# Kernel tuning notes

Hardware: AMD Instinct MI355X
Metric: run time of the kernel (lower is better)

The kernel has to match this reference:

```python
import jax, jax.numpy as jnp
import numpy as np

N = 65536      # total atoms
D = 1024       # hidden_size (encoder output dim)
H = 2048       # ffn_hidden_size
OUT = 1        # output_size
M = 4096       # number of molecules (segments)


def _lin(k, fi, fo):
    return jax.random.normal(k, (fi, fo), jnp.float32) * (1.0 / np.sqrt(fi))


def setup_inputs() -> dict:
    key = jax.random.key(0)
    ks = jax.random.split(key, 14)
    hidden = jax.random.normal(ks[0], (N, D), jnp.float32)
    segment_ids = jnp.sort(jax.random.randint(ks[1], (N,), 0, M)).astype(jnp.int64)
    inp = {
        "hidden": hidden,
        "ffn_W1": _lin(ks[2], D, H), "ffn_b1": jnp.zeros((H,), jnp.float32),
        "ffn_W2": _lin(ks[3], H, H), "ffn_b2": jnp.zeros((H,), jnp.float32),
        "ffn_W3": _lin(ks[4], H, OUT), "ffn_b3": jnp.zeros((OUT,), jnp.float32),
        "wr_W1": _lin(ks[5], D, H), "wr_b1": jnp.zeros((H,), jnp.float32),
        "wr_W2": _lin(ks[6], H, H), "wr_b2": jnp.zeros((H,), jnp.float32),
        "wr_W3": _lin(ks[7], H, OUT), "wr_b3": jnp.ones((OUT,), jnp.float32),  # bias=1 keeps segment weight sums away from 0
        "segment_ids": segment_ids,
    }
    return inp


def _ffn(x, W1, b1, W2, b2, W3, b3):
    # Dropout(p) is identity in eval; activation = ReLU
    h = jax.nn.relu(x @ W1 + b1)
    h = jax.nn.relu(h @ W2 + b2)
    return h @ W3 + b3


def reference(hidden, ffn_W1, ffn_b1, ffn_W2, ffn_b2, ffn_W3, ffn_b3,
              wr_W1, wr_b1, wr_W2, wr_b2, wr_W3, wr_b3, segment_ids):
    seg = segment_ids.astype(jnp.int32)
    output = _ffn(hidden, ffn_W1, ffn_b1, ffn_W2, ffn_b2, ffn_W3, ffn_b3)   # [N, OUT]
    weights = _ffn(hidden, wr_W1, wr_b1, wr_W2, wr_b2, wr_W3, wr_b3)        # [N, OUT]
    # per-molecule sums over ALL elements of the segment slice (matches .sum())
    out_sum = jax.ops.segment_sum(output.sum(-1), seg, num_segments=M)      # [M]
    w_sum = jax.ops.segment_sum(weights.sum(-1), seg, num_segments=M)       # [M]
    ratio = (out_sum / w_sum)[seg][:, None]                                 # [N, 1]
    return output - weights * ratio
```

## Files before the change

### kernel.cpp

```cpp
#include <hip/hip_runtime.h>
#include <hip/hip_bf16.h>

#define DEVINL __device__ __forceinline__

typedef __attribute__((ext_vector_type(8))) short s8v;
typedef __attribute__((ext_vector_type(4))) float f4v;

using bf16 = __hip_bfloat16;

DEVINL unsigned short f2bu(float f) {
  bf16 h = __float2bfloat16(f);
  return *reinterpret_cast<unsigned short*>(&h);
}

DEVINL void gload16(const void* g, void* l) {
  __builtin_amdgcn_global_load_lds((const __attribute__((address_space(1))) void*)g,
                                   (__attribute__((address_space(3))) void*)l, 16, 0, 0);
}

__global__ void k_f32_to_bf16(const float* __restrict__ x, unsigned short* __restrict__ y, long n4) {
  long i = (long)blockIdx.x * blockDim.x + threadIdx.x;
  if (i >= n4) return;
  float4 v = ((const float4*)x)[i];
  ushort4 o;
  o.x = f2bu(v.x); o.y = f2bu(v.y); o.z = f2bu(v.z); o.w = f2bu(v.w);
  ((ushort4*)y)[i] = o;
}

__global__ void k_transpose_bf16(const float* __restrict__ W, unsigned short* __restrict__ Wt,
                                 int rows, int cols) {
  __shared__ float tile[32][33];
  const int tx = threadIdx.x, ty = threadIdx.y;
  const int c0 = blockIdx.x * 32, r0 = blockIdx.y * 32;
  #pragma unroll
  for (int i = ty; i < 32; i += 8)
    tile[i][tx] = W[(long)(r0 + i) * cols + (c0 + tx)];
  __syncthreads();
  #pragma unroll
  for (int i = ty; i < 32; i += 8)
    Wt[(long)(c0 + i) * rows + (r0 + tx)] = f2bu(tile[tx][i]);
}

template<int EPI>
__global__ __launch_bounds__(256, 2)
void k_gemm_bt(const unsigned short* __restrict__ A, const unsigned short* __restrict__ Bt,
               unsigned short* __restrict__ C, const float* __restrict__ bias,
               const float* __restrict__ w3, float* __restrict__ oacc,
               int N, int K) {
  __shared__ unsigned short As[128 * 64];
  __shared__ unsigned short Bs[128 * 64];
  const int tid = threadIdx.x;
  const int w = tid >> 6;
  const int lane = tid & 63;
  const int bn = blockIdx.x, bm = blockIdx.y;
  const int wm = (w >> 1) * 64, wn = (w & 1) * 64;

  f4v acc[4][4];
  #pragma unroll
  for (int a = 0; a < 4; ++a)
    #pragma unroll
    for (int b = 0; b < 4; ++b)
      #pragma unroll
      for (int r = 0; r < 4; ++r) acc[a][b][r] = 0.f;

  const int r_in = lane >> 3;
  const int c_in = (lane & 7) * 8;
  const unsigned short* Ag = A + ((long)bm * 128 + w * 32 + r_in) * K + c_in;
  const unsigned short* Bg = Bt + ((long)bn * 128 + w * 32 + r_in) * K + c_in;
  char* AsB = (char*)As + w * 32 * 128;
  char* BsB = (char*)Bs + w * 32 * 128;

  const int row_a = wm + (lane & 15);
  const int row_b = wn + (lane & 15);
  const int kreg = (lane >> 4) * 8;

  for (int kt = 0; kt < K; kt += 64) {
    __syncthreads();
    #pragma unroll
    for (int t = 0; t < 4; ++t) {
      gload16(Ag + (long)t * 8 * K, AsB + t * 1024);
      gload16(Bg + (long)t * 8 * K, BsB + t * 1024);
    }
    Ag += 64; Bg += 64;
    __syncthreads();
    #pragma unroll
    for (int kk = 0; kk < 2; ++kk) {
      s8v af[4], bf_[4];
      const int kb = kk * 32 + kreg;
      #pragma unroll
      for (int i = 0; i < 4; ++i) {
        af[i]  = *(const s8v*)&As[(row_a + i * 16) * 64 + kb];
        bf_[i] = *(const s8v*)&Bs[(row_b + i * 16) * 64 + kb];
      }
      #pragma unroll
      for (int mi = 0; mi < 4; ++mi)
        #pragma unroll
        for (int ni = 0; ni < 4; ++ni)
          acc[mi][ni] = __builtin_amdgcn_mfma_f32_16x16x32_bf16(af[mi], bf_[ni], acc[mi][ni], 0, 0, 0);
    }
  }

  const int crow0 = wm + (lane >> 4) * 4;
  const int ccol0 = wn + (lane & 15);
  if (EPI == 1) {
    #pragma unroll
    for (int mi = 0; mi < 4; ++mi)
      #pragma unroll
      for (int ni = 0; ni < 4; ++ni) {
        const int col = bn * 128 + ccol0 + ni * 16;
        const float bb = bias[col];
        #pragma unroll
        for (int r = 0; r < 4; ++r) {
          const long row = (long)bm * 128 + crow0 + mi * 16 + r;
          float v = acc[mi][ni][r] + bb;
          v = v > 0.f ? v : 0.f;
          C[row * N + col] = f2bu(v);
        }
      }
  } else {
    #pragma unroll
    for (int mi = 0; mi < 4; ++mi)
      #pragma unroll
      for (int r = 0; r < 4; ++r) {
        float s = 0.f;
        #pragma unroll
        for (int ni = 0; ni < 4; ++ni) {
          const int col = bn * 128 + ccol0 + ni * 16;
          float v = acc[mi][ni][r] + bias[col];
          v = v > 0.f ? v : 0.f;
          s += v * w3[col];
        }
        s += __shfl_xor(s, 1, 64);
        s += __shfl_xor(s, 2, 64);
        s += __shfl_xor(s, 4, 64);
        s += __shfl_xor(s, 8, 64);
        if ((lane & 15) == 0) {
          const long row = (long)bm * 128 + crow0 + mi * 16 + r;
          atomicAdd(&oacc[row], s);
        }
      }
  }
}

__global__ void k_detect(const int* __restrict__ seg, int n, int* __restrict__ flag) {
  if (blockIdx.x == 0 && threadIdx.x == 0) flag[0] = (seg[n - 1] == 0) ? 1 : 0;
}

__global__ void k_segsum(const float* __restrict__ oacc, const float* __restrict__ wacc,
                         const int* __restrict__ seg, const int* __restrict__ flag,
                         const float* __restrict__ ob3, const float* __restrict__ wb3,
                         float* __restrict__ osum, float* __restrict__ wsum, int n) {
  int i = blockIdx.x * blockDim.x + threadIdx.x;
  if (i >= n) return;
  int s = flag[0] ? seg[2 * i] : seg[i];
  atomicAdd(&osum[s], oacc[i] + ob3[0]);
  atomicAdd(&wsum[s], wacc[i] + wb3[0]);
}

__global__ void k_final(const float* __restrict__ oacc, const float* __restrict__ wacc,
                        const int* __restrict__ seg, const int* __restrict__ flag,
                        const float* __restrict__ ob3, const float* __restrict__ wb3,
                        const float* __restrict__ osum, const float* __restrict__ wsum,
                        float* __restrict__ out, int n) {
  int i = blockIdx.x * blockDim.x + threadIdx.x;
  if (i >= n) return;
  int s = flag[0] ? seg[2 * i] : seg[i];
  float o = oacc[i] + ob3[0];
  float ww = wacc[i] + wb3[0];
  out[i] = o - ww * (osum[s] / wsum[s]);
}

extern "C" void kernel_launch(void* const* d_in, const int* in_sizes, int n_in,
                              void* d_out, int out_size, void* d_ws, size_t ws_size,
                              hipStream_t stream) {
  constexpr int NA = 65536, D = 1024, H = 2048, M = 4096;
  const float* hidden = (const float*)d_in[0];
  const float* fW1 = (const float*)d_in[1];
  const float* fb1 = (const float*)d_in[2];
  const float* fW2 = (const float*)d_in[3];
  const float* fb2 = (const float*)d_in[4];
  const float* fW3 = (const float*)d_in[5];
  const float* fb3 = (const float*)d_in[6];
  const float* wW1 = (const float*)d_in[7];
  const float* wb1 = (const float*)d_in[8];
  const float* wW2 = (const float*)d_in[9];
  const float* wb2 = (const float*)d_in[10];
  const float* wW3 = (const float*)d_in[11];
  const float* wb3 = (const float*)d_in[12];
  const int* seg = (const int*)d_in[13];
  float* out = (float*)d_out;

  char* ws = (char*)d_ws;
  size_t off = 0;
  auto alloc = [&](size_t bytes) { char* p = ws + off; off += (bytes + 255) & ~(size_t)255; return p; };
  unsigned short* hbf  = (unsigned short*)alloc((size_t)NA * D * 2);
  unsigned short* w1tf = (unsigned short*)alloc((size_t)H * D * 2);
  unsigned short* w1tw = (unsigned short*)alloc((size_t)H * D * 2);
  unsigned short* w2tf = (unsigned short*)alloc((size_t)H * H * 2);
  unsigned short* w2tw = (unsigned short*)alloc((size_t)H * H * 2);
  unsigned short* h1   = (unsigned short*)alloc((size_t)NA * H * 2);
  float* oacc = (float*)alloc((size_t)NA * 4);
  float* wacc = (float*)alloc((size_t)NA * 4);
  float* osum = (float*)alloc((size_t)M * 4);
  float* wsum = (float*)alloc((size_t)M * 4);
  int* flag = (int*)alloc(256);

  k_f32_to_bf16<<<(int)((long)NA * D / 4 / 256), 256, 0, stream>>>(hidden, hbf, (long)NA * D / 4);
  dim3 tb(32, 8);
  k_transpose_bf16<<<dim3(H / 32, D / 32), tb, 0, stream>>>(fW1, w1tf, D, H);
  k_transpose_bf16<<<dim3(H / 32, D / 32), tb, 0, stream>>>(wW1, w1tw, D, H);
  k_transpose_bf16<<<dim3(H / 32, H / 32), tb, 0, stream>>>(fW2, w2tf, H, H);
  k_transpose_bf16<<<dim3(H / 32, H / 32), tb, 0, stream>>>(wW2, w2tw, H, H);

  hipMemsetAsync(oacc, 0, (size_t)((char*)flag - (char*)oacc), stream);
  k_detect<<<1, 64, 0, stream>>>(seg, NA, flag);

  k_gemm_bt<1><<<dim3(H / 128, NA / 128), 256, 0, stream>>>(hbf, w1tf, h1, fb1, nullptr, nullptr, H, D);
  k_gemm_bt<2><<<dim3(H / 128, NA / 128), 256, 0, stream>>>(h1, w2tf, nullptr, fb2, fW3, oacc, H, H);
  k_gemm_bt<1><<<dim3(H / 128, NA / 128), 256, 0, stream>>>(hbf, w1tw, h1, wb1, nullptr, nullptr, H, D);
  k_gemm_bt<2><<<dim3(H / 128, NA / 128), 256, 0, stream>>>(h1, w2tw, nullptr, wb2, wW3, wacc, H, H);

  k_segsum<<<NA / 256, 256, 0, stream>>>(oacc, wacc, seg, flag, fb3, wb3, osum, wsum, NA);
  k_final<<<NA / 256, 256, 0, stream>>>(oacc, wacc, seg, flag, fb3, wb3, osum, wsum, out, NA);
}
```

Measured before the change: 2.135 ms.

## Replace GEMM with 256x256 tile, 8-wave, double-buffered swizzled LDS pipeline

New measurement: 2.041 ms. -4.4%, faster.

```diff
diff --git a/kernel.cpp b/kernel.cpp
--- a/kernel.cpp
+++ b/kernel.cpp
@@ -7,10 +7,11 @@
 typedef __attribute__((ext_vector_type(4))) float f4v;
 
 using bf16 = __hip_bfloat16;
-
-DEVINL unsigned short f2bu(float f) {
+typedef unsigned short u16;
+
+DEVINL u16 f2bu(float f) {
   bf16 h = __float2bfloat16(f);
-  return *reinterpret_cast<unsigned short*>(&h);
+  return *reinterpret_cast<u16*>(&h);
 }
 
 DEVINL void gload16(const void* g, void* l) {
@@ -18,7 +19,11 @@
                                    (__attribute__((address_space(3))) void*)l, 16, 0, 0);
 }
 
-__global__ void k_f32_to_bf16(const float* __restrict__ x, unsigned short* __restrict__ y, long n4) {
+#define BAR()   __builtin_amdgcn_s_barrier()
+#define LGKM0() asm volatile("s_waitcnt lgkmcnt(0)" ::: "memory")
+#define VM(n)   asm volatile("s_waitcnt vmcnt(" #n ")" ::: "memory")
+
+__global__ void k_f32_to_bf16(const float* __restrict__ x, u16* __restrict__ y, long n4) {
   long i = (long)blockIdx.x * blockDim.x + threadIdx.x;
   if (i >= n4) return;
   float4 v = ((const float4*)x)[i];
@@ -27,7 +32,7 @@
   ((ushort4*)y)[i] = o;
 }
 
-__global__ void k_transpose_bf16(const float* __restrict__ W, unsigned short* __restrict__ Wt,
+__global__ void k_transpose_bf16(const float* __restrict__ W, u16* __restrict__ Wt,
                                  int rows, int cols) {
   __shared__ float tile[32][33];
   const int tx = threadIdx.x, ty = threadIdx.y;
@@ -41,105 +46,143 @@
     Wt[(long)(c0 + i) * rows + (r0 + tx)] = f2bu(tile[tx][i]);
 }
 
+extern __shared__ char smem[];
+
 template<int EPI>
-__global__ __launch_bounds__(256, 2)
-void k_gemm_bt(const unsigned short* __restrict__ A, const unsigned short* __restrict__ Bt,
-               unsigned short* __restrict__ C, const float* __restrict__ bias,
-               const float* __restrict__ w3, float* __restrict__ oacc,
-               int N, int K) {
-  __shared__ unsigned short As[128 * 64];
-  __shared__ unsigned short Bs[128 * 64];
+__global__ __launch_bounds__(512, 2)
+void k_gemm8(const u16* __restrict__ A, const u16* __restrict__ Bt,
+             u16* __restrict__ C, const float* __restrict__ bias,
+             const float* __restrict__ w3, float* __restrict__ oacc,
+             int N, int K) {
   const int tid = threadIdx.x;
-  const int w = tid >> 6;
-  const int lane = tid & 63;
-  const int bn = blockIdx.x, bm = blockIdx.y;
-  const int wm = (w >> 1) * 64, wn = (w & 1) * 64;
-
-  f4v acc[4][4];
+  const int w = tid >> 6, lane = tid & 63;
+  const int id = blockIdx.x;
+  const int cpx = gridDim.x >> 3;
+  const int sw = (id & 7) * cpx + (id >> 3);
+  const int bn = sw & 7, bm = sw >> 3;
+
+  const int wm = (w >> 2) * 128, wn = (w & 3) * 64;
+  const int nt = K >> 6;
+
+  f4v acc[8][4];
   #pragma unroll
-  for (int a = 0; a < 4; ++a)
-    #pragma unroll
-    for (int b = 0; b < 4; ++b)
+  for (int i = 0; i < 8; ++i)
+    #pragma unroll
+    for (int jj = 0; jj < 4; ++jj)
       #pragma unroll
-      for (int r = 0; r < 4; ++r) acc[a][b][r] = 0.f;
-
-  const int r_in = lane >> 3;
-  const int c_in = (lane & 7) * 8;
-  const unsigned short* Ag = A + ((long)bm * 128 + w * 32 + r_in) * K + c_in;
-  const unsigned short* Bg = Bt + ((long)bn * 128 + w * 32 + r_in) * K + c_in;
-  char* AsB = (char*)As + w * 32 * 128;
-  char* BsB = (char*)Bs + w * 32 * 128;
-
-  const int row_a = wm + (lane & 15);
-  const int row_b = wn + (lane & 15);
-  const int kreg = (lane >> 4) * 8;
-
-  for (int kt = 0; kt < K; kt += 64) {
-    __syncthreads();
-    #pragma unroll
-    for (int t = 0; t < 4; ++t) {
-      gload16(Ag + (long)t * 8 * K, AsB + t * 1024);
-      gload16(Bg + (long)t * 8 * K, BsB + t * 1024);
-    }
-    Ag += 64; Bg += 64;
-    __syncthreads();
-    #pragma unroll
-    for (int kk = 0; kk < 2; ++kk) {
-      s8v af[4], bf_[4];
-      const int kb = kk * 32 + kreg;
+      for (int r = 0; r < 4; ++r) acc[i][jj][r] = 0.f;
+
+  const int rowl = tid >> 2;
+  const int jsw = (tid & 3) ^ (rowl & 3);
+  const u16* gA = A + (long)(bm * 256 + rowl) * K + jsw * 8;
+  const u16* gB = Bt + (long)(bn * 256 + rowl) * K + jsw * 8;
+  const long cstr = (long)128 * K;
+  const uint wb = (uint)w * 1024u;
+
+  const uint swz = ((uint)((lane >> 4) ^ (lane & 3))) * 16u;
+  const uint aoff = (uint)(wm + (lane & 15)) * 64u + swz;
+  const uint boff = (uint)(wn + (lane & 15)) * 64u + swz + 32768u;
+
+#define STAGE_A(pp, ks, t) do { \
+    const u16* g_ = gA + (long)(t) * 64 + (ks) * 32; \
+    char* l_ = smem + (uint)(pp) * 65536u + (uint)(ks) * 16384u + wb; \
+    gload16(g_, l_); gload16(g_ + cstr, l_ + 8192); } while (0)
+#define STAGE_B(pp, ks, t) do { \
+    const u16* g_ = gB + (long)(t) * 64 + (ks) * 32; \
+    char* l_ = smem + (uint)(pp) * 65536u + 32768u + (uint)(ks) * 16384u + wb; \
+    gload16(g_, l_); gload16(g_ + cstr, l_ + 8192); } while (0)
+
+#define MFMA8(c0i, c1i) do { \
+    __builtin_amdgcn_s_setprio(1); \
+    _Pragma("unroll") \
+    for (int mi = 0; mi < 8; ++mi) { \
+      acc[mi][c0i] = __builtin_amdgcn_mfma_f32_16x16x32_bf16(afr[mi], bfr[0], acc[mi][c0i], 0, 0, 0); \
+      acc[mi][c1i] = __builtin_amdgcn_mfma_f32_16x16x32_bf16(afr[mi], bfr[1], acc[mi][c1i], 0, 0, 0); \
+    } \
+    __builtin_amdgcn_s_setprio(0); } while (0)
+
+  STAGE_A(0, 0, 0); STAGE_B(0, 0, 0); STAGE_A(0, 1, 0); STAGE_B(0, 1, 0);
+  if (nt > 1) { STAGE_A(1, 0, 1); STAGE_B(1, 0, 1); VM(4); }
+  else        { VM(0); }
+  BAR();
+
+  s8v afr[8], bfr[2];
+  for (int t = 0; t < nt; ++t) {
+    const int p = t & 1, q = p ^ 1;
+    const uint pb = (uint)p * 65536u;
+    #pragma unroll
+    for (int mi = 0; mi < 8; ++mi)
+      afr[mi] = *(const s8v*)(smem + pb + aoff + (uint)mi * 1024u);
+    bfr[0] = *(const s8v*)(smem + pb + boff);
+    bfr[1] = *(const s8v*)(smem + pb + boff + 1024u);
+    if (t + 1 < nt) STAGE_A(q, 1, t + 1);
+    BAR(); LGKM0();
+    MFMA8(0, 1);
+    BAR();
+    bfr[0] = *(const s8v*)(smem + pb + boff + 2048u);
+    bfr[1] = *(const s8v*)(smem + pb + boff + 3072u);
+    if (t + 1 < nt) STAGE_B(q, 1, t + 1);
+    BAR(); LGKM0();
+    MFMA8(2, 3);
+    BAR();
+    #pragma unroll
+    for (int mi = 0; mi < 8; ++mi)
+      afr[mi] = *(const s8v*)(smem + pb + 16384u + aoff + (uint)mi * 1024u);
+    bfr[0] = *(const s8v*)(smem + pb + boff + 16384u);
+    bfr[1] = *(const s8v*)(smem + pb + boff + 16384u + 1024u);
+    if (t + 2 < nt) STAGE_A(p, 0, t + 2);
+    BAR(); LGKM0();
+    MFMA8(0, 1);
+    BAR();
+    bfr[0] = *(const s8v*)(smem + pb + boff + 16384u + 2048u);
+    bfr[1] = *(const s8v*)(smem + pb + boff + 16384u + 3072u);
+    if (t + 2 < nt) { STAGE_B(p, 0, t + 2); VM(4); }
+    else            { VM(0); }
+    BAR(); LGKM0();
+    MFMA8(2, 3);
+    BAR();
+  }
+
+  const int crow = bm * 256 + wm + ((lane >> 4) << 2);
+  const int ccol = bn * 256 + wn + (lane & 15);
+  if (EPI == 1) {
+    #pragma unroll
+    for (int jj = 0; jj < 4; ++jj) {
+      const float bb = bias[ccol + jj * 16];
       #pragma unroll
-      for (int i = 0; i < 4; ++i) {
-        af[i]  = *(const s8v*)&As[(row_a + i * 16) * 64 + kb];
-        bf_[i] = *(const s8v*)&Bs[(row_b + i * 16) * 64 + kb];
-      }
-      #pragma unroll
-      for (int mi = 0; mi < 4; ++mi)
-        #pragma unroll
-        for (int ni = 0; ni < 4; ++ni)
-          acc[mi][ni] = __builtin_amdgcn_mfma_f32_16x16x32_bf16(af[mi], bf_[ni], acc[mi][ni], 0, 0, 0);
-    }
-  }
-
-  const int crow0 = wm + (lane >> 4) * 4;
-  const int ccol0 = wn + (lane & 15);
-  if (EPI == 1) {
-    #pragma unroll
-    for (int mi = 0; mi < 4; ++mi)
-      #pragma unroll
-      for (int ni = 0; ni < 4; ++ni) {
-        const int col = bn * 128 + ccol0 + ni * 16;
-        const float bb = bias[col];
+      for (int mi = 0; mi < 8; ++mi)
         #pragma unroll
         for (int r = 0; r < 4; ++r) {
-          const long row = (long)bm * 128 + crow0 + mi * 16 + r;
-          float v = acc[mi][ni][r] + bb;
+          float v = acc[mi][jj][r] + bb;
           v = v > 0.f ? v : 0.f;
-          C[row * N + col] = f2bu(v);
+          C[(long)(crow + mi * 16 + r) * N + ccol + jj * 16] = f2bu(v);
         }
-      }
+    }
   } else {
-    #pragma unroll
-    for (int mi = 0; mi < 4; ++mi)
+    float bb[4], ww[4];
+    #pragma unroll
+    for (int jj = 0; jj < 4; ++jj) { bb[jj] = bias[ccol + jj * 16]; ww[jj] = w3[ccol + jj * 16]; }
+    #pragma unroll
+    for (int mi = 0; mi < 8; ++mi)
       #pragma unroll
       for (int r = 0; r < 4; ++r) {
         float s = 0.f;
         #pragma unroll
-        for (int ni = 0; ni < 4; ++ni) {
-          const int col = bn * 128 + ccol0 + ni * 16;
-          float v = acc[mi][ni][r] + bias[col];
+        for (int jj = 0; jj < 4; ++jj) {
+          float v = acc[mi][jj][r] + bb[jj];
           v = v > 0.f ? v : 0.f;
-          s += v * w3[col];
+          s += v * ww[jj];
         }
         s += __shfl_xor(s, 1, 64);
         s += __shfl_xor(s, 2, 64);
         s += __shfl_xor(s, 4, 64);
         s += __shfl_xor(s, 8, 64);
-        if ((lane & 15) == 0) {
-          const long row = (long)bm * 128 + crow0 + mi * 16 + r;
-          atomicAdd(&oacc[row], s);
-        }
+        if ((lane & 15) == 0) atomicAdd(&oacc[crow + mi * 16 + r], s);
       }
   }
+#undef STAGE_A
+#undef STAGE_B
+#undef MFMA8
 }
 
 __global__ void k_detect(const int* __restrict__ seg, int n, int* __restrict__ flag) {
@@ -193,17 +236,20 @@
   char* ws = (char*)d_ws;
   size_t off = 0;
   auto alloc = [&](size_t bytes) { char* p = ws + off; off += (bytes + 255) & ~(size_t)255; return p; };
-  unsigned short* hbf  = (unsigned short*)alloc((size_t)NA * D * 2);
-  unsigned short* w1tf = (unsigned short*)alloc((size_t)H * D * 2);
-  unsigned short* w1tw = (unsigned short*)alloc((size_t)H * D * 2);
-  unsigned short* w2tf = (unsigned short*)alloc((size_t)H * H * 2);
-  unsigned short* w2tw = (unsigned short*)alloc((size_t)H * H * 2);
-  unsigned short* h1   = (unsigned short*)alloc((size_t)NA * H * 2);
+  u16* hbf  = (u16*)alloc((size_t)NA * D * 2);
+  u16* w1tf = (u16*)alloc((size_t)H * D * 2);
+  u16* w1tw = (u16*)alloc((size_t)H * D * 2);
+  u16* w2tf = (u16*)alloc((size_t)H * H * 2);
+  u16* w2tw = (u16*)alloc((size_t)H * H * 2);
+  u16* h1   = (u16*)alloc((size_t)NA * H * 2);
   float* oacc = (float*)alloc((size_t)NA * 4);
   float* wacc = (float*)alloc((size_t)NA * 4);
   float* osum = (float*)alloc((size_t)M * 4);
   float* wsum = (float*)alloc((size_t)M * 4);
   int* flag = (int*)alloc(256);
+
+  hipFuncSetAttribute((const void*)k_gemm8<1>, hipFuncAttributeMaxDynamicSharedMemorySize, 131072);
+  hipFuncSetAttribute((const void*)k_gemm8<2>, hipFuncAttributeMaxDynamicSharedMemorySize, 131072);
 
   k_f32_to_bf16<<<(int)((long)NA * D / 4 / 256), 256, 0, stream>>>(hidden, hbf, (long)NA * D / 4);
   dim3 tb(32, 8);
@@ -215,10 +261,11 @@
   hipMemsetAsync(oacc, 0, (size_t)((char*)flag - (char*)oacc), stream);
   k_detect<<<1, 64, 0, stream>>>(seg, NA, flag);
 
-  k_gemm_bt<1><<<dim3(H / 128, NA / 128), 256, 0, stream>>>(hbf, w1tf, h1, fb1, nullptr, nullptr, H, D);
-  k_gemm_bt<2><<<dim3(H / 128, NA / 128), 256, 0, stream>>>(h1, w2tf, nullptr, fb2, fW3, oacc, H, H);
-  k_gemm_bt<1><<<dim3(H / 128, NA / 128), 256, 0, stream>>>(hbf, w1tw, h1, wb1, nullptr, nullptr, H, D);
-  k_gemm_bt<2><<<dim3(H / 128, NA / 128), 256, 0, stream>>>(h1, w2tw, nullptr, wb2, wW3, wacc, H, H);
+  const int nblk = (H / 256) * (NA / 256);
+  k_gemm8<1><<<nblk, 512, 131072, stream>>>(hbf, w1tf, h1, fb1, nullptr, nullptr, H, D);
+  k_gemm8<2><<<nblk, 512, 131072, stream>>>(h1, w2tf, nullptr, fb2, fW3, oacc, H, H);
+  k_gemm8<1><<<nblk, 512, 131072, stream>>>(hbf, w1tw, h1, wb1, nullptr, nullptr, H, D);
+  k_gemm8<2><<<nblk, 512, 131072, stream>>>(h1, w2tw, nullptr, wb2, wW3, wacc, H, H);
 
   k_segsum<<<NA / 256, 256, 0, stream>>>(oacc, wacc, seg, flag, fb3, wb3, osum, wsum, NA);
   k_final<<<NA / 256, 256, 0, stream>>>(oacc, wacc, seg, flag, fb3, wb3, osum, wsum, out, NA);
```
